# Kernel optimization log

Hardware: AMD Instinct MI355X
Metric: run time of the kernel (lower is better)

Reference implementation:

```python
import jax, jax.numpy as jnp
from jax import lax
import numpy as np

B = 256
# conv stack: (in_ch, out_ch, kernel)
_CONV_CFG = [(1, 3, 4), (3, 9, 4), (9, 12, 4), (12, 15, 4), (15, 15, 3)]
_FLAT = 15 * 4 ** 4  # 3840, matches nn.Linear(15*(18-14)**4, 100)


def _conv4d(x, w, b):
    """True 4D valid convolution. x: [B,C,d1,d2,d3,d4], w: [O,I,k,k,k,k]."""
    dn = lax.conv_dimension_numbers(x.shape, w.shape, ('NCDHWX', 'OIDHWX', 'NCDHWX'))
    y = lax.conv_general_dilated(x, w, window_strides=(1, 1, 1, 1),
                                 padding='VALID', dimension_numbers=dn)
    return y + b.reshape((1, -1) + (1,) * 4)


def setup_inputs() -> dict:
    key = jax.random.key(0)
    ks = jax.random.split(key, 16)
    inp = {'x': jax.random.normal(ks[0], (B, 1, 18, 18, 18, 18), dtype=jnp.float32)}
    for i, (ci, co, k) in enumerate(_CONV_CFG, start=1):
        fan_in = ci * k ** 4
        inp[f'w{i}'] = jax.random.normal(ks[2 * i - 1], (co, ci, k, k, k, k), dtype=jnp.float32) / np.sqrt(fan_in)
        inp[f'b{i}'] = jnp.zeros((co,), dtype=jnp.float32)
    inp['fc1_w'] = jax.random.normal(ks[11], (_FLAT, 100), dtype=jnp.float32) / np.sqrt(_FLAT)
    inp['fc1_b'] = jnp.zeros((100,), dtype=jnp.float32)
    inp['fc2_w'] = jax.random.normal(ks[12], (100, 1), dtype=jnp.float32) / np.sqrt(100.0)
    inp['fc2_b'] = jnp.zeros((1,), dtype=jnp.float32)
    return inp


def reference(x, w1, b1, w2, b2, w3, b3, w4, b4, w5, b5, fc1_w, fc1_b, fc2_w, fc2_b):
    h = jax.nn.relu(_conv4d(x, w1, b1))
    h = jax.nn.relu(_conv4d(h, w2, b2))
    h = jax.nn.relu(_conv4d(h, w3, b3))
    h = jax.nn.relu(_conv4d(h, w4, b4))
    h = jax.nn.relu(_conv4d(h, w5, b5))  # [B,15,4,4,4,4]
    h = h.reshape(h.shape[0], -1)        # [B,3840], torch Flatten order
    # Dropout(0.5) is identity at inference (eval mode)
    h = jax.nn.relu(h @ fc1_w + fc1_b)
    return jax.nn.sigmoid(h @ fc2_w + fc2_b)  # [B,1]
```

## Files before the change

kernel.cpp:

```cpp
#include <hip/hip_runtime.h>
#include <hip/hip_bf16.h>


#define BATCH 256
typedef unsigned int u32;
typedef float    f32x4  __attribute__((ext_vector_type(4)));
typedef float    f32x16 __attribute__((ext_vector_type(16)));
typedef _Float16 f16x8  __attribute__((ext_vector_type(8)));

struct __attribute__((packed, aligned(4))) f16x8w { f16x8 v; };

__global__ void cvt_f32_f16_pair(const float* __restrict__ in,
                                 _Float16* __restrict__ o,
                                 _Float16* __restrict__ os, int n8) {
    int i = blockIdx.x * blockDim.x + threadIdx.x;
    if (i >= n8) return;
    const f32x4* p = (const f32x4*)(in + (size_t)i * 8);
    f32x4 a = p[0], b = p[1];
    float c = (i + 1 < n8) ? in[(size_t)i * 8 + 8] : 0.0f;
    f16x8 v, vs;
    #pragma unroll
    for (int j = 0; j < 4; ++j) { v[j] = (_Float16)a[j]; v[4 + j] = (_Float16)b[j]; }
    #pragma unroll
    for (int j = 0; j < 7; ++j) vs[j] = v[j + 1];
    vs[7] = (_Float16)c;
    *(f16x8*)(o  + (size_t)i * 8) = v;
    *(f16x8*)(os + (size_t)i * 8) = vs;
}

__device__ __forceinline__ _Float16 conv_wf_elem(const float* __restrict__ w,
        int e, int COUT, int CIN, int KS, int S) {
    int j    = e & 7;
    int lane = (e >> 3) & 63;
    int st   = e >> 9;
    int k1 = st % KS;
    int r1 = st / KS;
    int k3p = r1 & 1;
    int r2  = r1 >> 1;
    int k2 = r2 % KS;
    int ci = r2 / KS;
    int gg = lane >> 5, col = lane & 31;
    int oc = col / S, s = col % S;
    int k3 = k3p * 2 + gg;
    int k4 = j - s;
    float v = 0.0f;
    if (oc < COUT && k3 < KS && k4 >= 0 && k4 < KS)
        v = w[((((oc * CIN + ci) * KS + k1) * KS + k2) * KS + k3) * KS + k4];
    return (_Float16)v;
}

__global__ void prepack_all(const float* __restrict__ w1, const float* __restrict__ w2,
                            const float* __restrict__ w3, const float* __restrict__ w4,
                            const float* __restrict__ w5, const float* __restrict__ fw,
                            _Float16* __restrict__ wf1, _Float16* __restrict__ wf2,
                            _Float16* __restrict__ wf3, _Float16* __restrict__ wf4,
                            _Float16* __restrict__ wf5, _Float16* __restrict__ wfc) {
    int idx = blockIdx.x * 256 + threadIdx.x;
    if (idx < 16384)  { wf1[idx] = conv_wf_elem(w1, idx, 3, 1, 4, 5);  return; }
    idx -= 16384;
    if (idx < 49152)  { wf2[idx] = conv_wf_elem(w2, idx, 9, 3, 4, 3);  return; }
    idx -= 49152;
    if (idx < 147456) { wf3[idx] = conv_wf_elem(w3, idx, 12, 9, 4, 2); return; }
    idx -= 147456;
    if (idx < 196608) { wf4[idx] = conv_wf_elem(w4, idx, 15, 12, 4, 2); return; }
    idx -= 196608;
    if (idx < 138240) { wf5[idx] = conv_wf_elem(w5, idx, 15, 15, 3, 2); return; }
    idx -= 138240;
    if (idx < 430080) {
        int j    = idx & 7;
        int lane = (idx >> 3) & 63;
        int t9   = idx >> 9;
        int st   = t9 % 120;
        int ni   = t9 / 120;
        int k    = st * 32 + (lane >> 4) * 8 + j;
        int col  = ni * 16 + (lane & 15);
        wfc[idx] = (_Float16)((col < 100) ? fw[k * 100 + col] : 0.0f);
    }
}

template<int BYTES>
__device__ __forceinline__ void stage_b(const _Float16* gsrc, char* ldst, int tid) {
    constexpr int N16 = BYTES / 16;
    const int wv = tid >> 6, ln = tid & 63;
    #pragma unroll
    for (int it = 0; it * 256 < N16; ++it) {
        int u16 = it * 256 + (wv << 6);
        if (u16 < N16) {
            const char* gp = (const char*)gsrc + (size_t)(u16 + ln) * 16;
            __builtin_amdgcn_global_load_lds(
                (const __attribute__((address_space(1))) unsigned int*)gp,
                (__attribute__((address_space(3))) unsigned int*)(ldst + u16 * 16),
                16, 0, 0);
        }
    }
}

template<int CIN, int COUT, int KS, int DIN, int DP, int S, int OP, int T,
         int CG, int MINW, int SODD, int WSHIFT>
__launch_bounds__(256, MINW)
__global__ void conv4d_v14(const _Float16* __restrict__ x,
                           const _Float16* __restrict__ xs,
                           const _Float16* __restrict__ wf,
                           const float* __restrict__ bias,
                           _Float16* __restrict__ out,
                           _Float16* __restrict__ outs) {
    constexpr int DOUT = DIN - KS + 1;
    constexpr int NB   = (DOUT + S - 1) / S;
    constexpr int PCOL = DOUT * DOUT * NB;
    constexpr int NTC  = (PCOL + 31) / 32;
    constexpr int NG   = DOUT / T;
    static_assert(DOUT % T == 0, "T must divide DOUT");
    constexpr int XD2 = DIN * DP;
    constexpr int XD1 = DIN * XD2;
    constexpr int XCI = DIN * XD1;
    constexpr int GROUPS = CIN * KS * 2;
    static_assert(GROUPS % CG == 0, "CG must divide GROUPS");
    constexpr int CSTEPS = CG * KS;
    constexpr int CBYTES = CSTEPS * 1024;
    constexpr int NCHUNK = GROUPS / CG;
    constexpr int NBUF   = (NCHUNK > 1) ? 2 : 1;
    constexpr int AJ = T + KS - 1;
    constexpr int W  = T + 1;
    constexpr u32 NW   = (u32)BATCH * NG * NTC;
    constexpr u32 POUT = (u32)DOUT * DOUT * DOUT * OP;

    __shared__ char bsm[NBUF * CBYTES];
    const int tid = threadIdx.x;
    u32 wid = blockIdx.x * 4u + (u32)(tid >> 6);
    if (wid >= NW) wid = NW - 1u;
    const int ln = tid & 63;
    const int g  = ln >> 5;
    const int r  = ln & 31;

    u32 tc = wid % (u32)NTC;  u32 q = wid / (u32)NTC;
    u32 d1g = q % (u32)NG;    u32 b = q / (u32)NG;
    u32 rr = tc * 32u + (u32)r;  if (rr >= (u32)PCOL) rr = (u32)PCOL - 1u;
    u32 u  = rr % (u32)NB;    u32 q2 = rr / (u32)NB;
    u32 d3 = q2 % (u32)DOUT;  u32 d2 = q2 / (u32)DOUT;

    const u32 o = b * (u32)(CIN * XCI) + d1g * (u32)(T * XD1)
                + d2 * (u32)XD2 + d3 * (u32)DP + (u32)(g * DP) + u * (u32)S;
    const char* xb;
    if (SODD) {
        u32 p = o & 1u;
        xb = p ? ((const char*)xs + (size_t)(o - 1u) * 2)
               : ((const char*)x  + (size_t)o * 2);
    } else {
        xb = (const char*)x + (size_t)o * 2;
    }

    f32x16 acc[T];
    #pragma unroll
    for (int t = 0; t < T; ++t)
        #pragma unroll
        for (int i = 0; i < 16; ++i) acc[t][i] = 0.0f;

    stage_b<CBYTES>(wf, &bsm[0], tid);

    #pragma unroll 1
    for (int ch = 0; ch < NCHUNK; ++ch) {
        __syncthreads();
        if (NCHUNK > 1 && ch + 1 < NCHUNK)
            stage_b<CBYTES>(wf + (size_t)(ch + 1) * CSTEPS * 512,
                            &bsm[((ch + 1) & 1) * CBYTES], tid);
        const char* bb = &bsm[(ch & 1) * (NBUF > 1 ? CBYTES : 0)] + ln * 16;
        #pragma unroll
        for (int gi = 0; gi < CG; ++gi) {
            int grp = ch * CG + gi;
            int k3p = grp & 1;
            int k2  = (grp >> 1) % KS;
            int ci  = (grp >> 1) / KS;
            u32 goff = ((u32)ci * (u32)XCI + (u32)k2 * (u32)XD2
                      + (u32)(k3p * 2 * DP)) * 2u;
            const char* ap = xb + goff;

            f16x8 ar[W];
            #pragma unroll
            for (int j = 0; j < T; ++j)
                ar[j] = ((const f16x8w*)(ap + j * (XD1 * 2)))->v;
            #pragma unroll
            for (int k1 = 0; k1 < KS; ++k1) {
                if (T + k1 < AJ)
                    ar[(T + k1) % W] = ((const f16x8w*)(ap + (T + k1) * (XD1 * 2)))->v;
                f16x8 bf = *(const f16x8*)(bb + (gi * KS + k1) * 1024);
                __builtin_amdgcn_s_setprio(1);
                #pragma unroll
                for (int t = 0; t < T; ++t)
                    acc[t] = __builtin_amdgcn_mfma_f32_32x32x16_f16(
                        ar[(k1 + t) % W], bf, acc[t], 0, 0, 0);
                __builtin_amdgcn_s_setprio(0);
            }
        }
    }

    const int oc = r / S, s = r % S;
    if (oc >= COUT) return;
    float bv = bias[oc];
    #pragma unroll
    for (int reg = 0; reg < 16; ++reg) {
        int rowoff = (reg & 3) + 8 * (reg >> 2) + 4 * g;
        u32 rr2 = tc * 32u + (u32)rowoff;
        if (rr2 >= (u32)PCOL) rr2 = (u32)PCOL - 1u;
        u32 uu = rr2 % (u32)NB;  u32 qq = rr2 / (u32)NB;
        u32 dd3 = qq % (u32)DOUT; u32 dd2 = qq / (u32)DOUT;
        u32 d4 = uu * (u32)S + (u32)s;
        if (d4 < (u32)DOUT) {
            u32 obase = (b * (u32)COUT + (u32)oc) * POUT
                      + (dd2 * (u32)DOUT + dd3) * (u32)OP + d4
                      + d1g * (u32)(T * DOUT * DOUT * OP);
            #pragma unroll
            for (int t = 0; t < T; ++t) {
                u32 oidx = obase + (u32)t * (u32)(DOUT * DOUT * OP);
                _Float16 v = (_Float16)fmaxf(acc[t][reg] + bv, 0.0f);
                out[oidx] = v;
                if (WSHIFT) { if (oidx >= 1u) outs[oidx - 1u] = v; }
            }
        }
    }
}

__launch_bounds__(256)
__global__ void fc1_mfma(const _Float16* __restrict__ h,
                         const _Float16* __restrict__ wfc,
                         const float* __restrict__ bias,
                         float* __restrict__ o) {
    int wv   = blockIdx.x * 4 + (threadIdx.x >> 6);
    int lane = threadIdx.x & 63;
    int r = lane & 15, g = lane >> 4;
    int mi = wv / 7, ni = wv % 7;
    const f16x8* A  = (const f16x8*)(h + (size_t)(mi * 16 + r) * 3840);
    const f16x8* Bv = (const f16x8*)wfc;
    f32x4 acc = {0.f, 0.f, 0.f, 0.f};
    #pragma unroll 4
    for (int st = 0; st < 120; ++st) {
        f16x8 a = A[st * 4 + g];
        f16x8 b = Bv[(ni * 120 + st) * 64 + lane];
        acc = __builtin_amdgcn_mfma_f32_16x16x32_f16(a, b, acc, 0, 0, 0);
    }
    int col = ni * 16 + r;
    if (col < 100) {
        float bv = bias[col];
        #pragma unroll
        for (int i = 0; i < 4; ++i) {
            int row = mi * 16 + g * 4 + i;
            o[row * 100 + col] = fmaxf(acc[i] + bv, 0.0f);
        }
    }
}

__global__ void fc2_sigmoid(const float* __restrict__ h,
                            const float* __restrict__ w,
                            const float* __restrict__ bias,
                            float* __restrict__ out) {
    int b = blockIdx.x * blockDim.x + threadIdx.x;
    if (b >= BATCH) return;
    const float* hb = h + b * 100;
    float acc = bias[0];
    #pragma unroll
    for (int j = 0; j < 100; ++j)
        acc = fmaf(hb[j], w[j], acc);
    out[b] = 1.0f / (1.0f + expf(-acc));
}

extern "C" void kernel_launch(void* const* d_in, const int* in_sizes, int n_in,
                              void* d_out, int out_size, void* d_ws, size_t ws_size,
                              hipStream_t stream) {
    const float* x    = (const float*)d_in[0];
    const float* w1   = (const float*)d_in[1];
    const float* b1   = (const float*)d_in[2];
    const float* w2   = (const float*)d_in[3];
    const float* b2   = (const float*)d_in[4];
    const float* w3   = (const float*)d_in[5];
    const float* b3   = (const float*)d_in[6];
    const float* w4   = (const float*)d_in[7];
    const float* b4   = (const float*)d_in[8];
    const float* w5   = (const float*)d_in[9];
    const float* b5   = (const float*)d_in[10];
    const float* fc1w = (const float*)d_in[11];
    const float* fc1b = (const float*)d_in[12];
    const float* fc2w = (const float*)d_in[13];
    const float* fc2b = (const float*)d_in[14];
    float* out = (float*)d_out;

    _Float16* W = (_Float16*)d_ws;
    _Float16* x16  = W;
    _Float16* x16s = W + 26873856;
    _Float16* h1   = W + 53747712;
    _Float16* h1s  = W + 95219712;
    _Float16* h2   = W;
    _Float16* h3   = h1s;
    _Float16* h4   = h1s + 22394880;
    _Float16* h5   = h1s + 27371520;
    _Float16* wf1  = W + 136691712;
    _Float16* wf2  = W + 136708096;
    _Float16* wf3  = W + 136757248;
    _Float16* wf4  = W + 136904704;
    _Float16* wf5  = W + 137101312;
    _Float16* wfc  = W + 137239552;
    float* fc1out  = (float*)(W + 137669632);

    cvt_f32_f16_pair<<<13122, 256, 0, stream>>>(x, x16, x16s, 3359232);
    prepack_all<<<3820, 256, 0, stream>>>(w1, w2, w3, w4, w5, fc1w,
                                          wf1, wf2, wf3, wf4, wf5, wfc);

    conv4d_v14<1, 3, 4, 18, 18, 5, 16, 3, 8, 4, 1, 1>
        <<<7040, 256, 0, stream>>>(x16, x16s, wf1, b1, h1, h1s);
    conv4d_v14<3, 9, 4, 15, 16, 3, 12, 6, 4, 3, 1, 0>
        <<<2304, 256, 0, stream>>>(h1, h1s, wf2, b2, h2, h2);
    conv4d_v14<9, 12, 4, 12, 12, 2, 10, 3, 4, 4, 0, 0>
        <<<2496, 256, 0, stream>>>(h2, h2, wf3, b3, h3, h3);
    conv4d_v14<12, 15, 4, 9, 10, 2, 6, 3, 4, 4, 0, 0>
        <<<512, 256, 0, stream>>>(h3, h3, wf4, b4, h4, h4);
    conv4d_v14<15, 15, 3, 6, 6, 2, 4, 4, 6, 4, 0, 0>
        <<<64, 256, 0, stream>>>(h4, h4, wf5, b5, h5, h5);

    fc1_mfma<<<28, 256, 0, stream>>>(h5, wfc, fc1b, fc1out);
    fc2_sigmoid<<<1, 256, 0, stream>>>(fc1out, fc2w, fc2b, out);
}
```

Measured before the change: 865.6 us.

## Add LDS-staged double-buffered conv3 kernel using async global-to-LDS loads

```diff
diff --git a/kernel.cpp b/kernel.cpp
--- a/kernel.cpp
+++ b/kernel.cpp
@@ -219,6 +219,130 @@
     }
 }
 
+__launch_bounds__(256, 4)
+__global__ void conv3_ldsA(const _Float16* __restrict__ x,
+                           const _Float16* __restrict__ wf,
+                           const float* __restrict__ bias,
+                           _Float16* __restrict__ out) {
+    constexpr int CIN = 9, DIN = 12, DP = 12, DOUT = 9, S = 2, NB = 5;
+    constexpr int COUT = 12, T = 3, KS = 4, OP = 10;
+    constexpr int XD2 = DIN * DP;
+    constexpr int XD1 = DIN * XD2;
+    constexpr int XCI = DIN * XD1;
+    constexpr int PCOL = 405, NTC = 13, NG = 3;
+    constexpr int PLANE = DIN * DP * 2 / DIN;
+    constexpr int PL = DIN * 24;
+    constexpr int D2W = 7;
+    constexpr int SLAB = D2W * PL;
+    constexpr int N16 = 756;
+    constexpr int BUFS = 12288;
+    constexpr u32 POUT = (u32)DOUT * DOUT * DOUT * OP;
+    (void)PLANE;
+
+    __shared__ char am[2 * BUFS + 64];
+    const int tid = threadIdx.x;
+    const int ln = tid & 63, wv = tid >> 6;
+    const int g = ln >> 5, r = ln & 31;
+
+    u32 blk = blockIdx.x;
+    u32 blkloc = blk & 3u;
+    u32 bd = blk >> 2;
+    u32 d1g = bd % (u32)NG;
+    u32 b   = bd / (u32)NG;
+    int tc = (int)(blkloc * 4u + (u32)wv); if (tc > NTC - 1) tc = NTC - 1;
+    u32 rr = (u32)tc * 32u + (u32)r; if (rr >= (u32)PCOL) rr = (u32)PCOL - 1u;
+    u32 u  = rr % (u32)NB;  u32 q2 = rr / (u32)NB;
+    u32 d3 = q2 % (u32)DOUT; u32 d2 = q2 / (u32)DOUT;
+    u32 d2a = (blkloc * 128u) / 45u; if (d2a > (u32)(DIN - D2W)) d2a = DIN - D2W;
+    u32 d2loc = d2 - d2a;
+
+    const u32 lanelds = d2loc * (u32)PL + d3 * 24u + u * 4u + (u32)g * 24u;
+
+    const char* xgb = (const char*)x
+        + ((size_t)b * CIN * XCI + (size_t)d1g * T * XD1 + (size_t)d2a * XD2) * 2;
+
+    const f16x8* wfv = (const f16x8*)wf;
+
+    f32x16 acc[T];
+    #pragma unroll
+    for (int t = 0; t < T; ++t)
+        #pragma unroll
+        for (int i = 0; i < 16; ++i) acc[t][i] = 0.0f;
+
+    auto stageA = [&](int ci, int parity) {
+        const char* src = xgb + (size_t)ci * XCI * 2;
+        char* dst = &am[parity * BUFS];
+        #pragma unroll
+        for (int it = 0; it < 3; ++it) {
+            int ugb = it * 256 + (wv << 6);
+            if (ugb < N16) {
+                int ug  = ugb + ln;
+                int d1p = ug / 126;
+                int rem = ug - d1p * 126;
+                const char* gp = src + (size_t)d1p * (XD1 * 2) + (size_t)rem * 16;
+                __builtin_amdgcn_global_load_lds(
+                    (const __attribute__((address_space(1))) unsigned int*)gp,
+                    (__attribute__((address_space(3))) unsigned int*)(dst + (size_t)ugb * 16),
+                    16, 0, 0);
+            }
+        }
+    };
+
+    stageA(0, 0);
+
+    #pragma unroll 1
+    for (int ci = 0; ci < CIN; ++ci) {
+        __syncthreads();
+        if (ci + 1 < CIN) stageA(ci + 1, (ci + 1) & 1);
+        const char* abase = &am[(ci & 1) * BUFS] + lanelds;
+        #pragma unroll
+        for (int k3p = 0; k3p < 2; ++k3p) {
+            #pragma unroll
+            for (int k2 = 0; k2 < KS; ++k2) {
+                f16x8 bf4[KS];
+                #pragma unroll
+                for (int k1 = 0; k1 < KS; ++k1)
+                    bf4[k1] = wfv[(size_t)((((ci * KS + k2) * 2 + k3p) * KS + k1)) * 64 + ln];
+                f16x8 ar[6];
+                #pragma unroll
+                for (int j = 0; j < 6; ++j)
+                    ar[j] = ((const f16x8w*)(abase + j * SLAB + k2 * PL + k3p * 48))->v;
+                #pragma unroll
+                for (int k1 = 0; k1 < KS; ++k1) {
+                    __builtin_amdgcn_s_setprio(1);
+                    #pragma unroll
+                    for (int t = 0; t < T; ++t)
+                        acc[t] = __builtin_amdgcn_mfma_f32_32x32x16_f16(
+                            ar[k1 + t], bf4[k1], acc[t], 0, 0, 0);
+                    __builtin_amdgcn_s_setprio(0);
+                }
+            }
+        }
+    }
+
+    const int oc = r / S, s = r % S;
+    if (oc >= COUT) return;
+    float bv = bias[oc];
+    #pragma unroll
+    for (int reg = 0; reg < 16; ++reg) {
+        int rowoff = (reg & 3) + 8 * (reg >> 2) + 4 * g;
+        u32 rr2 = (u32)tc * 32u + (u32)rowoff;
+        if (rr2 >= (u32)PCOL) rr2 = (u32)PCOL - 1u;
+        u32 uu = rr2 % (u32)NB;  u32 qq = rr2 / (u32)NB;
+        u32 dd3 = qq % (u32)DOUT; u32 dd2 = qq / (u32)DOUT;
+        u32 d4 = uu * (u32)S + (u32)s;
+        if (d4 < (u32)DOUT) {
+            u32 obase = (b * (u32)COUT + (u32)oc) * POUT
+                      + (dd2 * (u32)DOUT + dd3) * (u32)OP + d4
+                      + d1g * (u32)(T * DOUT * DOUT * OP);
+            #pragma unroll
+            for (int t = 0; t < T; ++t)
+                out[obase + (u32)t * (u32)(DOUT * DOUT * OP)]
+                    = (_Float16)fmaxf(acc[t][reg] + bv, 0.0f);
+        }
+    }
+}
+
 __launch_bounds__(256)
 __global__ void fc1_mfma(const _Float16* __restrict__ h,
                          const _Float16* __restrict__ wfc,
@@ -307,8 +431,7 @@
         <<<7040, 256, 0, stream>>>(x16, x16s, wf1, b1, h1, h1s);
     conv4d_v14<3, 9, 4, 15, 16, 3, 12, 6, 4, 3, 1, 0>
         <<<2304, 256, 0, stream>>>(h1, h1s, wf2, b2, h2, h2);
-    conv4d_v14<9, 12, 4, 12, 12, 2, 10, 3, 4, 4, 0, 0>
-        <<<2496, 256, 0, stream>>>(h2, h2, wf3, b3, h3, h3);
+    conv3_ldsA<<<3072, 256, 0, stream>>>(h2, wf3, b3, h3);
     conv4d_v14<12, 15, 4, 9, 10, 2, 6, 3, 4, 4, 0, 0>
         <<<512, 256, 0, stream>>>(h3, h3, wf4, b4, h4, h4);
     conv4d_v14<15, 15, 3, 6, 6, 2, 4, 4, 6, 4, 0, 0>
```

Result: slower. 906.5 us (+4.7%).

## Fuse fp32-to-fp16 input conversion into first conv and retune late-layer T

Applied to the files above, without the earlier changes.

```diff
diff --git a/kernel.cpp b/kernel.cpp
--- a/kernel.cpp
+++ b/kernel.cpp
@@ -9,24 +9,7 @@
 typedef _Float16 f16x8  __attribute__((ext_vector_type(8)));
 
 struct __attribute__((packed, aligned(4))) f16x8w { f16x8 v; };
-
-__global__ void cvt_f32_f16_pair(const float* __restrict__ in,
-                                 _Float16* __restrict__ o,
-                                 _Float16* __restrict__ os, int n8) {
-    int i = blockIdx.x * blockDim.x + threadIdx.x;
-    if (i >= n8) return;
-    const f32x4* p = (const f32x4*)(in + (size_t)i * 8);
-    f32x4 a = p[0], b = p[1];
-    float c = (i + 1 < n8) ? in[(size_t)i * 8 + 8] : 0.0f;
-    f16x8 v, vs;
-    #pragma unroll
-    for (int j = 0; j < 4; ++j) { v[j] = (_Float16)a[j]; v[4 + j] = (_Float16)b[j]; }
-    #pragma unroll
-    for (int j = 0; j < 7; ++j) vs[j] = v[j + 1];
-    vs[7] = (_Float16)c;
-    *(f16x8*)(o  + (size_t)i * 8) = v;
-    *(f16x8*)(os + (size_t)i * 8) = vs;
-}
+struct __attribute__((packed, aligned(4))) f32x4u { f32x4 v; };
 
 __device__ __forceinline__ _Float16 conv_wf_elem(const float* __restrict__ w,
         int e, int COUT, int CIN, int KS, int S) {
@@ -96,14 +79,15 @@
 }
 
 template<int CIN, int COUT, int KS, int DIN, int DP, int S, int OP, int T,
-         int CG, int MINW, int SODD, int WSHIFT>
+         int CG, int MINW, int FP32IN, int SODD, int WSHIFT>
 __launch_bounds__(256, MINW)
-__global__ void conv4d_v14(const _Float16* __restrict__ x,
-                           const _Float16* __restrict__ xs,
+__global__ void conv4d_v16(const void* __restrict__ xin,
+                           const void* __restrict__ xsin,
                            const _Float16* __restrict__ wf,
                            const float* __restrict__ bias,
                            _Float16* __restrict__ out,
                            _Float16* __restrict__ outs) {
+    constexpr int ES = FP32IN ? 4 : 2;
     constexpr int DOUT = DIN - KS + 1;
     constexpr int NB   = (DOUT + S - 1) / S;
     constexpr int PCOL = DOUT * DOUT * NB;
@@ -141,13 +125,31 @@
     const u32 o = b * (u32)(CIN * XCI) + d1g * (u32)(T * XD1)
                 + d2 * (u32)XD2 + d3 * (u32)DP + (u32)(g * DP) + u * (u32)S;
     const char* xb;
-    if (SODD) {
+    if (FP32IN) {
+        xb = (const char*)xin + (size_t)o * 4;
+    } else if (SODD) {
         u32 p = o & 1u;
-        xb = p ? ((const char*)xs + (size_t)(o - 1u) * 2)
-               : ((const char*)x  + (size_t)o * 2);
+        xb = p ? ((const char*)xsin + (size_t)(o - 1u) * 2)
+               : ((const char*)xin  + (size_t)o * 2);
     } else {
-        xb = (const char*)x + (size_t)o * 2;
-    }
+        xb = (const char*)xin + (size_t)o * 2;
+    }
+
+    auto load_frag = [&](const char* p) -> f16x8 {
+        if constexpr (FP32IN) {
+            f32x4 lo = ((const f32x4u*)p)->v;
+            f32x4 hi = ((const f32x4u*)(p + 16))->v;
+            f16x8 f;
+            #pragma unroll
+            for (int j = 0; j < 4; ++j) {
+                f[j]     = (_Float16)lo[j];
+                f[4 + j] = (_Float16)hi[j];
+            }
+            return f;
+        } else {
+            return ((const f16x8w*)p)->v;
+        }
+    };
 
     f32x16 acc[T];
     #pragma unroll
@@ -171,17 +173,17 @@
             int k2  = (grp >> 1) % KS;
             int ci  = (grp >> 1) / KS;
             u32 goff = ((u32)ci * (u32)XCI + (u32)k2 * (u32)XD2
-                      + (u32)(k3p * 2 * DP)) * 2u;
+                      + (u32)(k3p * 2 * DP)) * (u32)ES;
             const char* ap = xb + goff;
 
             f16x8 ar[W];
             #pragma unroll
             for (int j = 0; j < T; ++j)
-                ar[j] = ((const f16x8w*)(ap + j * (XD1 * 2)))->v;
+                ar[j] = load_frag(ap + j * (XD1 * ES));
             #pragma unroll
             for (int k1 = 0; k1 < KS; ++k1) {
                 if (T + k1 < AJ)
-                    ar[(T + k1) % W] = ((const f16x8w*)(ap + (T + k1) * (XD1 * 2)))->v;
+                    ar[(T + k1) % W] = load_frag(ap + (T + k1) * (XD1 * ES));
                 f16x8 bf = *(const f16x8*)(bb + (gi * KS + k1) * 1024);
                 __builtin_amdgcn_s_setprio(1);
                 #pragma unroll
@@ -283,36 +285,33 @@
     float* out = (float*)d_out;
 
     _Float16* W = (_Float16*)d_ws;
-    _Float16* x16  = W;
-    _Float16* x16s = W + 26873856;
-    _Float16* h1   = W + 53747712;
-    _Float16* h1s  = W + 95219712;
-    _Float16* h2   = W;
-    _Float16* h3   = h1s;
-    _Float16* h4   = h1s + 22394880;
-    _Float16* h5   = h1s + 27371520;
-    _Float16* wf1  = W + 136691712;
-    _Float16* wf2  = W + 136708096;
-    _Float16* wf3  = W + 136757248;
-    _Float16* wf4  = W + 136904704;
-    _Float16* wf5  = W + 137101312;
-    _Float16* wfc  = W + 137239552;
-    float* fc1out  = (float*)(W + 137669632);
-
-    cvt_f32_f16_pair<<<13122, 256, 0, stream>>>(x, x16, x16s, 3359232);
+    _Float16* h1   = W;
+    _Float16* h1s  = W + 41472000;
+    _Float16* h2   = W + 82944000;
+    _Float16* h3   = h1;
+    _Float16* h4   = h1 + 22394880;
+    _Float16* h5   = h1 + 27371520;
+    _Float16* wf1  = W + 130719744;
+    _Float16* wf2  = W + 130736128;
+    _Float16* wf3  = W + 130785280;
+    _Float16* wf4  = W + 130932736;
+    _Float16* wf5  = W + 131129344;
+    _Float16* wfc  = W + 131267584;
+    float* fc1out  = (float*)(W + 131697664);
+
     prepack_all<<<3820, 256, 0, stream>>>(w1, w2, w3, w4, w5, fc1w,
                                           wf1, wf2, wf3, wf4, wf5, wfc);
 
-    conv4d_v14<1, 3, 4, 18, 18, 5, 16, 3, 8, 4, 1, 1>
-        <<<7040, 256, 0, stream>>>(x16, x16s, wf1, b1, h1, h1s);
-    conv4d_v14<3, 9, 4, 15, 16, 3, 12, 6, 4, 3, 1, 0>
+    conv4d_v16<1, 3, 4, 18, 18, 5, 16, 3, 8, 4, 1, 0, 1>
+        <<<7040, 256, 0, stream>>>(x, x, wf1, b1, h1, h1s);
+    conv4d_v16<3, 9, 4, 15, 16, 3, 12, 6, 4, 3, 0, 1, 0>
         <<<2304, 256, 0, stream>>>(h1, h1s, wf2, b2, h2, h2);
-    conv4d_v14<9, 12, 4, 12, 12, 2, 10, 3, 4, 4, 0, 0>
+    conv4d_v16<9, 12, 4, 12, 12, 2, 10, 3, 4, 4, 0, 0, 0>
         <<<2496, 256, 0, stream>>>(h2, h2, wf3, b3, h3, h3);
-    conv4d_v14<12, 15, 4, 9, 10, 2, 6, 3, 4, 4, 0, 0>
-        <<<512, 256, 0, stream>>>(h3, h3, wf4, b4, h4, h4);
-    conv4d_v14<15, 15, 3, 6, 6, 2, 4, 4, 6, 4, 0, 0>
-        <<<64, 256, 0, stream>>>(h4, h4, wf5, b5, h5, h5);
+    conv4d_v16<12, 15, 4, 9, 10, 2, 6, 2, 4, 4, 0, 0, 0>
+        <<<768, 256, 0, stream>>>(h3, h3, wf4, b4, h4, h4);
+    conv4d_v16<15, 15, 3, 6, 6, 2, 4, 2, 6, 4, 0, 0, 0>
+        <<<128, 256, 0, stream>>>(h4, h4, wf5, b5, h5, h5);
 
     fc1_mfma<<<28, 256, 0, stream>>>(h5, wfc, fc1b, fc1out);
     fc2_sigmoid<<<1, 256, 0, stream>>>(fc1out, fc2w, fc2b, out);
```

Measured after the change: 859.2 us. About the same (-0.7%).
